# Kernel optimization log

Measured on AMD Instinct MI355X. Metric: run time of the kernel, lower is better.

## Reference

```python
import jax, jax.numpy as jnp
import numpy as np

EMBED_DIM = 1024
NUM_HEADS = 16
HEAD_DIM = EMBED_DIM // NUM_HEADS


def setup_inputs() -> dict:
    key = jax.random.key(0)
    ks = jax.random.split(key, 11)
    B, T, D = 4, 2048, EMBED_DIM
    s = 1.0 / np.sqrt(D)
    inp = {
        "x": jax.random.normal(ks[0], (B, T, D), dtype=jnp.float32),
        "wq": jax.random.normal(ks[1], (D, D), dtype=jnp.float32) * s,
        "bq": jnp.zeros((D,), dtype=jnp.float32),
        "wk": jax.random.normal(ks[2], (D, D), dtype=jnp.float32) * s,
        "bk": jnp.zeros((D,), dtype=jnp.float32),
        "wv": jax.random.normal(ks[3], (D, D), dtype=jnp.float32) * s,
        "bv": jnp.zeros((D,), dtype=jnp.float32),
        "wo": jax.random.normal(ks[4], (D, D), dtype=jnp.float32) * s,
        "bo": jnp.zeros((D,), dtype=jnp.float32),
        "ln_gamma": jnp.ones((D,), dtype=jnp.float32),
        "ln_beta": jnp.zeros((D,), dtype=jnp.float32),
    }
    return inp


def _attention(x, wq, bq, wk, bk, wv, bv, wo, bo, ln_gamma, ln_beta):
    B, T, D = x.shape
    H, Hd = NUM_HEADS, HEAD_DIM
    # projections -> (B, H, T, Hd)
    q = (x @ wq + bq).reshape(B, T, H, Hd).transpose(0, 2, 1, 3)
    k = (x @ wk + bk).reshape(B, T, H, Hd).transpose(0, 2, 1, 3)
    v = (x @ wv + bv).reshape(B, T, H, Hd).transpose(0, 2, 1, 3)
    scores = jnp.einsum("bhqd,bhkd->bhqk", q, k) / jnp.sqrt(jnp.asarray(Hd, x.dtype))
    attn = jax.nn.softmax(scores, axis=-1)  # dropout p=0 -> identity
    out = jnp.einsum("bhqk,bhkd->bhqd", attn, v)
    out = out.transpose(0, 2, 1, 3).reshape(B, T, D)
    out = out @ wo + bo
    # LayerNorm (no residual in the original forward)
    mu = jnp.mean(out, axis=-1, keepdims=True)
    var = jnp.var(out, axis=-1, keepdims=True)
    out = (out - mu) / jnp.sqrt(var + 1e-5) * ln_gamma + ln_beta
    return out


def reference(x, wq, bq, wk, bk, wv, bv, wo, bo, ln_gamma, ln_beta):
    return _attention(x, wq, bq, wk, bk, wv, bv, wo, bo, ln_gamma, ln_beta)
```

## Files before the change

### kernel.cpp

```cpp
#include <hip/hip_runtime.h>
#include <hip/hip_bf16.h>

typedef __bf16 bf16_t;
typedef __bf16 bf16x4v __attribute__((ext_vector_type(4)));
typedef __bf16 bf16x8 __attribute__((ext_vector_type(8)));
typedef float  f32x4  __attribute__((ext_vector_type(4)));

#define B_BATCH  4
#define T_SEQ    2048
#define D_MODEL  1024
#define N_HEADS  16
#define HEAD_DIM 64
#define M_ROWS   (B_BATCH * T_SEQ)

#define BM  128
#define BN  128
#define BKK 64
#define LDT 72

#define EXP2_SCALE 0.1803368801111204f

__global__ __launch_bounds__(256) void cvt_x(
    const float* __restrict__ in, bf16_t* __restrict__ out)
{
    const size_t i = ((size_t)blockIdx.x * 256 + threadIdx.x) * 4;
    const f32x4 v = *(const f32x4*)&in[i];
    bf16x4v o;
    for (int e = 0; e < 4; e++) o[e] = (bf16_t)v[e];
    *(bf16x4v*)&out[i] = o;
}

__global__ __launch_bounds__(256) void transpose_w(
    const float* __restrict__ w0, const float* __restrict__ w1,
    const float* __restrict__ w2, const float* __restrict__ w3,
    bf16_t* __restrict__ out)
{
    __shared__ bf16_t tile[32][33];
    const int z = blockIdx.z;
    const float* w = (z == 0) ? w0 : (z == 1) ? w1 : (z == 2) ? w2 : w3;
    bf16_t* o = out + (size_t)z * D_MODEL * D_MODEL;
    const int tx = threadIdx.x & 31, ty = threadIdx.x >> 5;
    const int k0 = blockIdx.y * 32, n0 = blockIdx.x * 32;
    for (int i = 0; i < 4; i++)
        tile[ty + i * 8][tx] = (bf16_t)w[(size_t)(k0 + ty + i * 8) * D_MODEL + n0 + tx];
    __syncthreads();
    for (int i = 0; i < 4; i++)
        o[(size_t)(n0 + ty + i * 8) * D_MODEL + k0 + tx] = tile[tx][ty + i * 8];
}

__global__ __launch_bounds__(256) void transpose_v(
    const bf16_t* __restrict__ V, bf16_t* __restrict__ VT)
{
    __shared__ bf16_t tile[32][33];
    const int bh = blockIdx.z;
    const bf16_t* src = V  + (size_t)bh * T_SEQ * HEAD_DIM;
    bf16_t*       dst = VT + (size_t)bh * T_SEQ * HEAD_DIM;
    const int tx = threadIdx.x & 31, ty = threadIdx.x >> 5;
    const int t0 = blockIdx.x * 32, d0 = blockIdx.y * 32;
    for (int i = 0; i < 4; i++)
        tile[ty + i * 8][tx] = src[(size_t)(t0 + ty + i * 8) * HEAD_DIM + d0 + tx];
    __syncthreads();
    for (int i = 0; i < 4; i++)
        dst[(size_t)(d0 + ty + i * 8) * T_SEQ + t0 + tx] = tile[tx][ty + i * 8];
}

template <int MODE>
__global__ __launch_bounds__(256) void gemm_k(
    const bf16_t* __restrict__ A, const bf16_t* __restrict__ wT_base,
    const float* __restrict__ b0, const float* __restrict__ b1,
    const float* __restrict__ b2, void* __restrict__ out_base)
{
    __shared__ __attribute__((aligned(16))) bf16_t As[BM][LDT];
    __shared__ __attribute__((aligned(16))) bf16_t Bs[BN][LDT];

    const int tid  = threadIdx.x;
    const int z    = blockIdx.z;
    const bf16_t* BT   = wT_base + (size_t)z * D_MODEL * D_MODEL;
    const float*  bias = (z == 0) ? b0 : (z == 1) ? b1 : b2;
    const int mbase = blockIdx.y * BM;
    const int nbase = blockIdx.x * BN;
    const int w = tid >> 6, lane = tid & 63, quad = lane >> 4, l16 = lane & 15;
    const int wm = (w & 1) * 64, wn = (w >> 1) * 64;

    f32x4 acc[4][4] = {};

    for (int kb = 0; kb < D_MODEL; kb += BKK) {
        __syncthreads();
        for (int it = 0; it < 4; it++) {
            int idx = it * 256 + tid;
            int r = idx >> 3, c8 = (idx & 7) * 8;
            *(bf16x8*)&As[r][c8] = *(const bf16x8*)&A [(size_t)(mbase + r) * D_MODEL + kb + c8];
            *(bf16x8*)&Bs[r][c8] = *(const bf16x8*)&BT[(size_t)(nbase + r) * D_MODEL + kb + c8];
        }
        __syncthreads();
        for (int s = 0; s < 2; s++) {
            bf16x8 af[4], bf[4];
            for (int i = 0; i < 4; i++)
                af[i] = *(const bf16x8*)&As[wm + i * 16 + l16][s * 32 + quad * 8];
            for (int j = 0; j < 4; j++)
                bf[j] = *(const bf16x8*)&Bs[wn + j * 16 + l16][s * 32 + quad * 8];
            for (int i = 0; i < 4; i++)
                for (int j = 0; j < 4; j++)
                    acc[i][j] = __builtin_amdgcn_mfma_f32_16x16x32_bf16(
                        af[i], bf[j], acc[i][j], 0, 0, 0);
        }
    }

    float bj[4];
    for (int j = 0; j < 4; j++)
        bj[j] = bias[nbase + wn + j * 16 + l16];

    for (int i = 0; i < 4; i++) {
        for (int r = 0; r < 4; r++) {
            const int rg = mbase + wm + i * 16 + quad * 4 + r;
            for (int j = 0; j < 4; j++) {
                const int cg = nbase + wn + j * 16 + l16;
                const float v = acc[i][j][r] + bj[j];
                if (MODE == 0) {
                    bf16_t* q = (bf16_t*)out_base + (size_t)z * ((size_t)M_ROWS * D_MODEL);
                    const int b = rg >> 11, t = rg & 2047, h = cg >> 6, hd = cg & 63;
                    q[(((size_t)(b * N_HEADS + h)) * T_SEQ + t) * HEAD_DIM + hd] = (bf16_t)v;
                } else {
                    ((float*)out_base)[(size_t)rg * D_MODEL + cg] = v;
                }
            }
        }
    }
}

__global__ __launch_bounds__(256, 4) void attn_k(
    const bf16_t* __restrict__ Q, const bf16_t* __restrict__ K,
    const bf16_t* __restrict__ VT, bf16_t* __restrict__ O)
{
    __shared__ __attribute__((aligned(16))) bf16_t Ks[64][LDT];
    __shared__ __attribute__((aligned(16))) bf16_t Vs[64][LDT];
    __shared__ __attribute__((aligned(16))) bf16_t Ps[4][32][LDT];

    const int tid = threadIdx.x;
    const int bh  = blockIdx.y;
    const int b = bh >> 4, h = bh & 15;
    const int qbase = blockIdx.x * 128;
    const int w = tid >> 6, lane = tid & 63, quad = lane >> 4, l16 = lane & 15;
    const size_t head_off = (size_t)bh * T_SEQ * HEAD_DIM;
    const bf16_t* Qh  = Q  + head_off;
    const bf16_t* Kh  = K  + head_off;
    const bf16_t* VTh = VT + head_off;

    bf16x8 bq[2][2];
    for (int iq = 0; iq < 2; iq++)
        for (int s = 0; s < 2; s++)
            bq[iq][s] = *(const bf16x8*)
                &Qh[(size_t)(qbase + w * 32 + iq * 16 + l16) * HEAD_DIM + s * 32 + quad * 8];

    float l_part[2] = {0.f, 0.f};
    f32x4 Oacc[2][4] = {};

    for (int kt = 0; kt < T_SEQ / 64; kt++) {
        const int kbase = kt * 64;
        __syncthreads();
        for (int it = 0; it < 2; it++) {
            int idx = it * 256 + tid;
            int r = idx >> 3, c8 = (idx & 7) * 8;
            *(bf16x8*)&Ks[r][c8] = *(const bf16x8*)&Kh [(size_t)(kbase + r) * HEAD_DIM + c8];
            *(bf16x8*)&Vs[r][c8] = *(const bf16x8*)&VTh[(size_t)r * T_SEQ + kbase + c8];
        }
        __syncthreads();

        f32x4 St[4][2] = {};
        for (int s = 0; s < 2; s++) {
            bf16x8 ak[4];
            for (int jk = 0; jk < 4; jk++)
                ak[jk] = *(const bf16x8*)&Ks[jk * 16 + l16][s * 32 + quad * 8];
            for (int jk = 0; jk < 4; jk++)
                for (int iq = 0; iq < 2; iq++)
                    St[jk][iq] = __builtin_amdgcn_mfma_f32_16x16x32_bf16(
                        ak[jk], bq[iq][s], St[jk][iq], 0, 0, 0);
        }

        for (int jk = 0; jk < 4; jk++)
            for (int iq = 0; iq < 2; iq++) {
                bf16x4v pv;
                for (int r = 0; r < 4; r++) {
                    const float p = __builtin_amdgcn_exp2f(St[jk][iq][r] * EXP2_SCALE);
                    l_part[iq] += p;
                    pv[r] = (bf16_t)p;
                }
                *(bf16x4v*)&Ps[w][iq * 16 + l16][jk * 16 + quad * 4] = pv;
            }
        asm volatile("" ::: "memory");

        for (int s = 0; s < 2; s++) {
            bf16x8 ap[2], bv[4];
            for (int iq = 0; iq < 2; iq++)
                ap[iq] = *(const bf16x8*)&Ps[w][iq * 16 + l16][s * 32 + quad * 8];
            for (int jn = 0; jn < 4; jn++)
                bv[jn] = *(const bf16x8*)&Vs[jn * 16 + l16][s * 32 + quad * 8];
            for (int iq = 0; iq < 2; iq++)
                for (int jn = 0; jn < 4; jn++)
                    Oacc[iq][jn] = __builtin_amdgcn_mfma_f32_16x16x32_bf16(
                        ap[iq], bv[jn], Oacc[iq][jn], 0, 0, 0);
        }
    }

    for (int iq = 0; iq < 2; iq++) {
        l_part[iq] += __shfl_xor(l_part[iq], 16, 64);
        l_part[iq] += __shfl_xor(l_part[iq], 32, 64);
    }

    for (int iq = 0; iq < 2; iq++) {
        for (int r = 0; r < 4; r++) {
            const int qrow = quad * 4 + r;
            const float inv = 1.f / __shfl(l_part[iq], qrow, 64);
            const int t = qbase + w * 32 + iq * 16 + qrow;
            for (int jn = 0; jn < 4; jn++) {
                const int hd = jn * 16 + l16;
                O[(((size_t)(b * T_SEQ + t)) * N_HEADS + h) * HEAD_DIM + hd] =
                    (bf16_t)(Oacc[iq][jn][r] * inv);
            }
        }
    }
}

__global__ __launch_bounds__(256) void ln_k(
    const float* __restrict__ proj, const float* __restrict__ gamma,
    const float* __restrict__ beta, float* __restrict__ out)
{
    __shared__ float red[4][2];
    const int row = blockIdx.x, tid = threadIdx.x;
    const float* p = proj + (size_t)row * D_MODEL + tid * 4;
    const f32x4 v = *(const f32x4*)p;
    float s1 = v[0] + v[1] + v[2] + v[3];
    float s2 = v[0] * v[0] + v[1] * v[1] + v[2] * v[2] + v[3] * v[3];
    for (int off = 32; off >= 1; off >>= 1) {
        s1 += __shfl_xor(s1, off, 64);
        s2 += __shfl_xor(s2, off, 64);
    }
    const int w = tid >> 6;
    if ((tid & 63) == 0) { red[w][0] = s1; red[w][1] = s2; }
    __syncthreads();
    const float S1 = red[0][0] + red[1][0] + red[2][0] + red[3][0];
    const float S2 = red[0][1] + red[1][1] + red[2][1] + red[3][1];
    const float mu  = S1 * (1.f / D_MODEL);
    const float var = S2 * (1.f / D_MODEL) - mu * mu;
    const float rstd = rsqrtf(var + 1e-5f);
    const int c = tid * 4;
    f32x4 o;
    for (int e = 0; e < 4; e++)
        o[e] = (v[e] - mu) * rstd * gamma[c + e] + beta[c + e];
    *(f32x4*)&out[(size_t)row * D_MODEL + c] = o;
}

extern "C" void kernel_launch(void* const* d_in, const int* in_sizes, int n_in,
                              void* d_out, int out_size, void* d_ws, size_t ws_size,
                              hipStream_t stream)
{
    const float* x  = (const float*)d_in[0];
    const float* wq = (const float*)d_in[1];
    const float* bq = (const float*)d_in[2];
    const float* wk = (const float*)d_in[3];
    const float* bk = (const float*)d_in[4];
    const float* wv = (const float*)d_in[5];
    const float* bv = (const float*)d_in[6];
    const float* wo = (const float*)d_in[7];
    const float* bo = (const float*)d_in[8];
    const float* g  = (const float*)d_in[9];
    const float* be = (const float*)d_in[10];

    char* ws = (char*)d_ws;
    bf16_t* xb   = (bf16_t*)(ws);
    bf16_t* wT   = (bf16_t*)(ws + ((size_t)16 << 20));
    bf16_t* qkv  = (bf16_t*)(ws + ((size_t)24 << 20));
    bf16_t* attn = (bf16_t*)(ws + ((size_t)72 << 20));
    float*  proj = (float*) (ws + ((size_t)88 << 20));
    bf16_t* vt   = (bf16_t*)proj;

    cvt_x<<<dim3(M_ROWS * D_MODEL / 1024), 256, 0, stream>>>(x, xb);
    transpose_w<<<dim3(32, 32, 4), 256, 0, stream>>>(wq, wk, wv, wo, wT);

    gemm_k<0><<<dim3(8, 64, 3), 256, 0, stream>>>(xb, wT, bq, bk, bv, (void*)qkv);

    bf16_t* Qm = qkv;
    bf16_t* Km = qkv + (size_t)M_ROWS * D_MODEL;
    bf16_t* Vm = Km + (size_t)M_ROWS * D_MODEL;

    transpose_v<<<dim3(64, 2, 64), 256, 0, stream>>>(Vm, vt);

    attn_k<<<dim3(16, 64), 256, 0, stream>>>(Qm, Km, vt, attn);

    gemm_k<1><<<dim3(8, 64, 1), 256, 0, stream>>>(
        attn, wT + (size_t)3 * D_MODEL * D_MODEL, bo, bo, bo, (void*)proj);

    ln_k<<<dim3(M_ROWS), 256, 0, stream>>>(proj, g, be, (float*)d_out);
}
```

Baseline: 334.5 us.

## Use direct global-to-LDS loads in GEMM and drop LDS staging in attention

The projection GEMM now fills its shared-memory tiles with global_load_lds, which copies global memory straight into LDS, and drops the padded row stride. The attention kernel no longer stages K and V^T through shared memory: each wave reads its MFMA operands directly from global memory, which also removes two block barriers per key tile. Attention blocks are remapped so that heads are grouped by XCD for L2 locality. The risks are LDS bank conflicts from the unpadded GEMM tiles and redundant global/L2 traffic, since all four waves now fetch the same K/V data separately.

```diff
diff --git a/kernel.cpp b/kernel.cpp
--- a/kernel.cpp
+++ b/kernel.cpp
@@ -5,6 +5,9 @@
 typedef __bf16 bf16x4v __attribute__((ext_vector_type(4)));
 typedef __bf16 bf16x8 __attribute__((ext_vector_type(8)));
 typedef float  f32x4  __attribute__((ext_vector_type(4)));
+
+typedef __attribute__((address_space(1))) void* gptr_t;
+typedef __attribute__((address_space(3))) void* lptr_t;
 
 #define B_BATCH  4
 #define T_SEQ    2048
@@ -70,8 +73,8 @@
     const float* __restrict__ b0, const float* __restrict__ b1,
     const float* __restrict__ b2, void* __restrict__ out_base)
 {
-    __shared__ __attribute__((aligned(16))) bf16_t As[BM][LDT];
-    __shared__ __attribute__((aligned(16))) bf16_t Bs[BN][LDT];
+    __shared__ __attribute__((aligned(16))) bf16_t As[BM][BKK];
+    __shared__ __attribute__((aligned(16))) bf16_t Bs[BN][BKK];
 
     const int tid  = threadIdx.x;
     const int z    = blockIdx.z;
@@ -81,16 +84,20 @@
     const int nbase = blockIdx.x * BN;
     const int w = tid >> 6, lane = tid & 63, quad = lane >> 4, l16 = lane & 15;
     const int wm = (w & 1) * 64, wn = (w >> 1) * 64;
+    const int lrow = lane >> 3, lcol = (lane & 7) * 8;
 
     f32x4 acc[4][4] = {};
 
     for (int kb = 0; kb < D_MODEL; kb += BKK) {
         __syncthreads();
         for (int it = 0; it < 4; it++) {
-            int idx = it * 256 + tid;
-            int r = idx >> 3, c8 = (idx & 7) * 8;
-            *(bf16x8*)&As[r][c8] = *(const bf16x8*)&A [(size_t)(mbase + r) * D_MODEL + kb + c8];
-            *(bf16x8*)&Bs[r][c8] = *(const bf16x8*)&BT[(size_t)(nbase + r) * D_MODEL + kb + c8];
+            const int r = w * 32 + it * 8;
+            __builtin_amdgcn_global_load_lds(
+                (gptr_t)&A [(size_t)(mbase + r + lrow) * D_MODEL + kb + lcol],
+                (lptr_t)&As[r][0], 16, 0, 0);
+            __builtin_amdgcn_global_load_lds(
+                (gptr_t)&BT[(size_t)(nbase + r + lrow) * D_MODEL + kb + lcol],
+                (lptr_t)&Bs[r][0], 16, 0, 0);
         }
         __syncthreads();
         for (int s = 0; s < 2; s++) {
@@ -132,14 +139,14 @@
     const bf16_t* __restrict__ Q, const bf16_t* __restrict__ K,
     const bf16_t* __restrict__ VT, bf16_t* __restrict__ O)
 {
-    __shared__ __attribute__((aligned(16))) bf16_t Ks[64][LDT];
-    __shared__ __attribute__((aligned(16))) bf16_t Vs[64][LDT];
     __shared__ __attribute__((aligned(16))) bf16_t Ps[4][32][LDT];
 
     const int tid = threadIdx.x;
-    const int bh  = blockIdx.y;
+    const int f = blockIdx.y * 16 + blockIdx.x;
+    const int xcd = f & 7, j = f >> 3;
+    const int bh = xcd * 8 + (j & 7);
+    const int qbase = (j >> 3) * 128;
     const int b = bh >> 4, h = bh & 15;
-    const int qbase = blockIdx.x * 128;
     const int w = tid >> 6, lane = tid & 63, quad = lane >> 4, l16 = lane & 15;
     const size_t head_off = (size_t)bh * T_SEQ * HEAD_DIM;
     const bf16_t* Qh  = Q  + head_off;
@@ -157,20 +164,13 @@
 
     for (int kt = 0; kt < T_SEQ / 64; kt++) {
         const int kbase = kt * 64;
-        __syncthreads();
-        for (int it = 0; it < 2; it++) {
-            int idx = it * 256 + tid;
-            int r = idx >> 3, c8 = (idx & 7) * 8;
-            *(bf16x8*)&Ks[r][c8] = *(const bf16x8*)&Kh [(size_t)(kbase + r) * HEAD_DIM + c8];
-            *(bf16x8*)&Vs[r][c8] = *(const bf16x8*)&VTh[(size_t)r * T_SEQ + kbase + c8];
-        }
-        __syncthreads();
 
         f32x4 St[4][2] = {};
         for (int s = 0; s < 2; s++) {
             bf16x8 ak[4];
             for (int jk = 0; jk < 4; jk++)
-                ak[jk] = *(const bf16x8*)&Ks[jk * 16 + l16][s * 32 + quad * 8];
+                ak[jk] = *(const bf16x8*)
+                    &Kh[(size_t)(kbase + jk * 16 + l16) * HEAD_DIM + s * 32 + quad * 8];
             for (int jk = 0; jk < 4; jk++)
                 for (int iq = 0; iq < 2; iq++)
                     St[jk][iq] = __builtin_amdgcn_mfma_f32_16x16x32_bf16(
@@ -194,7 +194,8 @@
             for (int iq = 0; iq < 2; iq++)
                 ap[iq] = *(const bf16x8*)&Ps[w][iq * 16 + l16][s * 32 + quad * 8];
             for (int jn = 0; jn < 4; jn++)
-                bv[jn] = *(const bf16x8*)&Vs[jn * 16 + l16][s * 32 + quad * 8];
+                bv[jn] = *(const bf16x8*)
+                    &VTh[(size_t)(jn * 16 + l16) * T_SEQ + kbase + s * 32 + quad * 8];
             for (int iq = 0; iq < 2; iq++)
                 for (int jn = 0; jn < 4; jn++)
                     Oacc[iq][jn] = __builtin_amdgcn_mfma_f32_16x16x32_bf16(
```

Measured after the change: 469.2 us. 1.4x slower.
